# Kernel tuning notes

Measured on AMD Instinct MI355X. Metric: run time of the kernel, lower is better.

## Reference

```python
import jax, jax.numpy as jnp
import numpy as np

EMB = 1024
HEADS = 16

def setup_inputs() -> dict:
    key = jax.random.key(0)
    ks = jax.random.split(key, 5)
    s = 1.0 / np.sqrt(EMB)
    x = jax.random.normal(ks[0], (2, 2048, EMB), dtype=jnp.float32)
    W_qkv = jax.random.normal(ks[1], (EMB, 3 * EMB), dtype=jnp.float32) * s
    b_qkv = jnp.zeros((3 * EMB,), dtype=jnp.float32)
    W_out = jax.random.normal(ks[2], (EMB, EMB), dtype=jnp.float32) * s
    b_out = jnp.zeros((EMB,), dtype=jnp.float32)
    return {"x": x, "W_qkv": W_qkv, "b_qkv": b_qkv, "W_out": W_out, "b_out": b_out}

def reference(x, W_qkv, b_qkv, W_out, b_out):
    B, N, C = x.shape
    H = HEADS
    D = C // H
    qkv = x @ W_qkv + b_qkv                      # [B,N,3C]
    qkv = qkv.reshape(B, N, 3, H, D)
    q, k, v = (qkv[:, :, i].transpose(0, 2, 1, 3) for i in range(3))  # [B,H,N,D]
    # NOTE: original scales by C**-0.5 (full embed dim), not head dim
    scale = C ** (-0.5)
    attn = jnp.einsum('bhnd,bhmd->bhnm', q, k) * scale
    attn = jax.nn.softmax(attn, axis=-1)
    out = jnp.einsum('bhnm,bhmd->bhnd', attn, v)  # [B,H,N,D]
    out = out.transpose(0, 2, 1, 3).reshape(B, N, C)
    return out @ W_out + b_out
```

## Files before the change

### kernel.cpp

```cpp
#include <hip/hip_runtime.h>
#include <hip/hip_bf16.h>
#include <cstdint>
#include <cstddef>

typedef __bf16 bf16;
typedef __bf16 bf16x4 __attribute__((ext_vector_type(4)));
typedef __bf16 bf16x8 __attribute__((ext_vector_type(8)));
typedef float f32x4 __attribute__((ext_vector_type(4)));
typedef float f32x16 __attribute__((ext_vector_type(16)));

#define LOG2E 1.4426950408889634f
#define QSCALE (0.03125f * LOG2E)

#define GLD16(gp, lp)                                                              \
  __builtin_amdgcn_global_load_lds((__attribute__((address_space(1))) void*)(gp),  \
                                   (__attribute__((address_space(3))) void*)(lp),  \
                                   16, 0, 0)

__global__ void k_prep(const float* __restrict__ x, const float* __restrict__ Wqkv,
                       const float* __restrict__ Wout, bf16* __restrict__ xb,
                       bf16* __restrict__ wqT, bf16* __restrict__ woT) {
  const int blk = blockIdx.x, tid = threadIdx.x;
  if (blk < 2048) {
    int i = (blk * 256 + tid) * 8;
    const float4* p = (const float4*)(x + i);
    float4 a = p[0], b = p[1];
    bf16x8 o;
    o[0] = (bf16)a.x; o[1] = (bf16)a.y; o[2] = (bf16)a.z; o[3] = (bf16)a.w;
    o[4] = (bf16)b.x; o[5] = (bf16)b.y; o[6] = (bf16)b.z; o[7] = (bf16)b.w;
    *(bf16x8*)(xb + i) = o;
    return;
  }
  const float* in;
  bf16* out;
  int R = 1024, C, bx, by;
  if (blk < 2048 + 3072) {
    in = Wqkv; out = wqT; C = 3072;
    bx = (blk - 2048) % 96; by = (blk - 2048) / 96;
  } else {
    in = Wout; out = woT; C = 1024;
    bx = (blk - 5120) % 32; by = (blk - 5120) / 32;
  }
  __shared__ float t[32][33];
  const int tx = tid & 31, ty = tid >> 5;
  int c0 = bx * 32, r0 = by * 32;
#pragma unroll
  for (int i = 0; i < 4; i++)
    t[ty + i * 8][tx] = in[(size_t)(r0 + ty + i * 8) * C + c0 + tx];
  __syncthreads();
#pragma unroll
  for (int i = 0; i < 4; i++)
    out[(size_t)(c0 + ty + i * 8) * R + r0 + tx] = (bf16)t[tx][ty + i * 8];
}

__global__ __launch_bounds__(256, 3) void k_gemm_qkv(
    const bf16* __restrict__ A, const bf16* __restrict__ Bt,
    const float* __restrict__ bias,
    bf16* __restrict__ qb, bf16* __restrict__ kb, bf16* __restrict__ vb) {
  __shared__ __align__(16) bf16 As[128 * 32];
  __shared__ __align__(16) bf16 Bs[128 * 32];
  const int tid = threadIdx.x;
  const int lane = tid & 63, w = tid >> 6;
  const int quad = lane >> 4, l16 = lane & 15;
  const int wm = (w >> 1) * 64, wn = (w & 1) * 64;
  const int bm = blockIdx.y * 128, bn = blockIdx.x * 128;
  f32x4 acc[4][4] = {};

  for (int kt = 0; kt < 1024; kt += 32) {
    __syncthreads();
#pragma unroll
    for (int p = 0; p < 2; p++) {
      int idx = p * 256 + tid;
      int row = idx >> 2, bq = idx & 3;
      int gb = (bq - ((row >> 1) & 3)) & 3;
      GLD16(A + (size_t)(bm + row) * 1024 + kt + gb * 8, As + idx * 8);
      GLD16(Bt + (size_t)(bn + row) * 1024 + kt + gb * 8, Bs + idx * 8);
    }
    __syncthreads();

    bf16x8 af[4], bfr[4];
#pragma unroll
    for (int mi = 0; mi < 4; mi++) {
      int row = wm + mi * 16 + l16;
      int bq = (quad + ((row >> 1) & 3)) & 3;
      af[mi] = *(const bf16x8*)(As + row * 32 + bq * 8);
    }
#pragma unroll
    for (int ni = 0; ni < 4; ni++) {
      int row = wn + ni * 16 + l16;
      int bq = (quad + ((row >> 1) & 3)) & 3;
      bfr[ni] = *(const bf16x8*)(Bs + row * 32 + bq * 8);
    }
#pragma unroll
    for (int mi = 0; mi < 4; mi++)
#pragma unroll
      for (int ni = 0; ni < 4; ni++)
        acc[mi][ni] =
            __builtin_amdgcn_mfma_f32_16x16x32_bf16(af[mi], bfr[ni], acc[mi][ni], 0, 0, 0);
  }

#pragma unroll
  for (int ni = 0; ni < 4; ni++) {
    int col = bn + wn + ni * 16 + l16;
    float bv = bias[col];
    int which = col >> 10, cc = col & 1023;
    int h = cc >> 6, d = cc & 63;
    if (which == 2) {
#pragma unroll
      for (int mi = 0; mi < 4; mi++) {
        int rowb = bm + wm + mi * 16 + quad * 4;
        int b = rowb >> 11, n0 = rowb & 2047;
        int n0p = (n0 & ~12) | ((n0 & 4) << 1) | ((n0 & 8) >> 1);
        bf16x4 vv;
#pragma unroll
        for (int r = 0; r < 4; r++) vv[r] = (bf16)(acc[mi][ni][r] + bv);
        *(bf16x4*)(vb + ((size_t)(b * 16 + h) * 64 + d) * 2048 + n0p) = vv;
      }
    } else {
#pragma unroll
      for (int mi = 0; mi < 4; mi++)
#pragma unroll
        for (int r = 0; r < 4; r++) {
          int row = bm + wm + mi * 16 + quad * 4 + r;
          int b = row >> 11, n = row & 2047;
          float v = acc[mi][ni][r] + bv;
          if (which == 0)
            qb[((size_t)(b * 16 + h) * 2048 + n) * 64 + d] = (bf16)(v * QSCALE);
          else
            kb[((size_t)(b * 16 + h) * 2048 + n) * 64 + d] = (bf16)v;
        }
    }
  }
}

__global__ __launch_bounds__(256, 2) void k_gemm_out(
    const bf16* __restrict__ A, const bf16* __restrict__ Bt,
    const float* __restrict__ bias, float* __restrict__ outF) {
  __shared__ __align__(16) bf16 As[64 * 32];
  __shared__ __align__(16) bf16 Bs[128 * 32];
  const int tid = threadIdx.x;
  const int lane = tid & 63, w = tid >> 6;
  const int quad = lane >> 4, l16 = lane & 15;
  const int wm = (w >> 1) * 32, wn = (w & 1) * 64;
  const int cid = (blockIdx.x & 7) * 64 + (blockIdx.x >> 3);
  const int bn = (cid & 7) * 128, bm = (cid >> 3) * 64;
  f32x4 acc[2][4] = {};

  for (int kt = 0; kt < 1024; kt += 32) {
    __syncthreads();
    {
      int idx = tid;
      int row = idx >> 2, bq = idx & 3;
      int gb = (bq - ((row >> 1) & 3)) & 3;
      GLD16(A + (size_t)(bm + row) * 1024 + kt + gb * 8, As + idx * 8);
    }
#pragma unroll
    for (int p = 0; p < 2; p++) {
      int idx = p * 256 + tid;
      int row = idx >> 2, bq = idx & 3;
      int gb = (bq - ((row >> 1) & 3)) & 3;
      GLD16(Bt + (size_t)(bn + row) * 1024 + kt + gb * 8, Bs + idx * 8);
    }
    __syncthreads();

    bf16x8 af[2], bfr[4];
#pragma unroll
    for (int mi = 0; mi < 2; mi++) {
      int row = wm + mi * 16 + l16;
      int bq = (quad + ((row >> 1) & 3)) & 3;
      af[mi] = *(const bf16x8*)(As + row * 32 + bq * 8);
    }
#pragma unroll
    for (int ni = 0; ni < 4; ni++) {
      int row = wn + ni * 16 + l16;
      int bq = (quad + ((row >> 1) & 3)) & 3;
      bfr[ni] = *(const bf16x8*)(Bs + row * 32 + bq * 8);
    }
#pragma unroll
    for (int mi = 0; mi < 2; mi++)
#pragma unroll
      for (int ni = 0; ni < 4; ni++)
        acc[mi][ni] =
            __builtin_amdgcn_mfma_f32_16x16x32_bf16(af[mi], bfr[ni], acc[mi][ni], 0, 0, 0);
  }

#pragma unroll
  for (int ni = 0; ni < 4; ni++) {
    int col = bn + wn + ni * 16 + l16;
    float bv = bias[col];
#pragma unroll
    for (int mi = 0; mi < 2; mi++)
#pragma unroll
      for (int r = 0; r < 4; r++) {
        int row = bm + wm + mi * 16 + quad * 4 + r;
        outF[(size_t)row * 1024 + col] = acc[mi][ni][r] + bv;
      }
  }
}

__global__ __launch_bounds__(256, 2) void k_flash(
    const bf16* __restrict__ Q, const bf16* __restrict__ K,
    const bf16* __restrict__ V, bf16* __restrict__ O) {
  __shared__ __align__(16) bf16 Kt[2][128 * 64];
  __shared__ __align__(16) bf16 Vt[2][64 * 128];
  const int tid = threadIdx.x;
  const int lane = tid & 63, w = tid >> 6;
  const int l31 = lane & 31, h = lane >> 5;
  const int x7 = l31 & 7;
  const int cid = ((blockIdx.x & 7) << 6) | (blockIdx.x >> 3);
  const int qt = cid & 15, bh = cid >> 4;
  const bf16* qh = Q + (size_t)bh * 2048 * 64;
  const bf16* kh = K + (size_t)bh * 2048 * 64;
  const bf16* vh = V + (size_t)bh * 64 * 2048;
  const int qrow = qt * 128 + w * 32 + l31;

  bf16x8 qf[4];
#pragma unroll
  for (int c4 = 0; c4 < 4; c4++)
    qf[c4] = *(const bf16x8*)(qh + (size_t)qrow * 64 + c4 * 16 + h * 8);

  bf16x8 ones;
#pragma unroll
  for (int j = 0; j < 8; j++) ones[j] = (bf16)1.0f;
  f32x16 z16 = {};

  f32x16 o0 = {}, o1 = {};
  f32x16 lacc = {};

  auto stage = [&](int kt2, int buf) {
#pragma unroll
    for (int pp = 0; pp < 4; pp++) {
      int idx = pp * 256 + tid;
      int row = idx >> 3, bq = idx & 7, gb = bq ^ (row & 7);
      GLD16(kh + (size_t)(kt2 * 128 + row) * 64 + gb * 8, &Kt[buf][idx * 8]);
    }
#pragma unroll
    for (int pp = 0; pp < 4; pp++) {
      int idx = pp * 256 + tid;
      int row = idx >> 4, bq = idx & 15, gb = bq ^ (row & 7);
      GLD16(vh + (size_t)row * 2048 + kt2 * 128 + gb * 8, &Vt[buf][idx * 8]);
    }
  };

  stage(0, 0);

  for (int t = 0; t < 16; t++) {
    const int p = t & 1;
    __syncthreads();
    if (t < 15) stage(t + 1, p ^ 1);
    const bf16* Kb = &Kt[p][0];
    const bf16* Vb = &Vt[p][0];

    f32x16 a[4];
    {
      __builtin_amdgcn_s_setprio(1);
#pragma unroll
      for (int c4 = 0; c4 < 4; c4++) {
        int off = ((2 * c4 + h) ^ x7) << 3;
#pragma unroll
        for (int g = 0; g < 4; g++) {
          bf16x8 kf = *(const bf16x8*)(Kb + (g * 32 + l31) * 64 + off);
          a[g] = __builtin_amdgcn_mfma_f32_32x32x16_bf16(kf, qf[c4], c4 ? a[g] : z16,
                                                         0, 0, 0);
        }
      }
      __builtin_amdgcn_s_setprio(0);
    }

    const bf16* v0 = Vb + l31 * 128;
    const bf16* v1 = v0 + 32 * 128;

#pragma unroll
    for (int g = 0; g < 4; g++) {
      bf16x8 pf0, pf1;
#pragma unroll
      for (int j = 0; j < 8; j++) {
        pf0[j] = (bf16)__builtin_amdgcn_exp2f(a[g][j]);
        pf1[j] = (bf16)__builtin_amdgcn_exp2f(a[g][8 + j]);
      }
      int e0 = ((4 * g + 0 + h) ^ x7) << 3;
      int e1 = ((4 * g + 2 + h) ^ x7) << 3;
      bf16x8 vf00 = *(const bf16x8*)(v0 + e0);
      bf16x8 vf10 = *(const bf16x8*)(v1 + e0);
      bf16x8 vf01 = *(const bf16x8*)(v0 + e1);
      bf16x8 vf11 = *(const bf16x8*)(v1 + e1);
      __builtin_amdgcn_s_setprio(1);
      lacc = __builtin_amdgcn_mfma_f32_32x32x16_bf16(ones, pf0, lacc, 0, 0, 0);
      o0 = __builtin_amdgcn_mfma_f32_32x32x16_bf16(vf00, pf0, o0, 0, 0, 0);
      o1 = __builtin_amdgcn_mfma_f32_32x32x16_bf16(vf10, pf0, o1, 0, 0, 0);
      lacc = __builtin_amdgcn_mfma_f32_32x32x16_bf16(ones, pf1, lacc, 0, 0, 0);
      o0 = __builtin_amdgcn_mfma_f32_32x32x16_bf16(vf01, pf1, o0, 0, 0, 0);
      o1 = __builtin_amdgcn_mfma_f32_32x32x16_bf16(vf11, pf1, o1, 0, 0, 0);
      __builtin_amdgcn_s_setprio(0);
    }
  }

  float inv = 1.0f / lacc[0];
  const int bb = bh >> 4, hh = bh & 15;
  bf16* orow = O + ((size_t)bb * 2048 + qrow) * 1024 + hh * 64;
#pragma unroll
  for (int g = 0; g < 4; g++) {
    bf16x4 ov0, ov1;
#pragma unroll
    for (int r = 0; r < 4; r++) {
      ov0[r] = (bf16)(o0[4 * g + r] * inv);
      ov1[r] = (bf16)(o1[4 * g + r] * inv);
    }
    *(bf16x4*)(orow + 8 * g + 4 * h) = ov0;
    *(bf16x4*)(orow + 32 + 8 * g + 4 * h) = ov1;
  }
}


extern "C" void kernel_launch(void* const* d_in, const int* in_sizes, int n_in,
                              void* d_out, int out_size, void* d_ws, size_t ws_size,
                              hipStream_t stream) {
  (void)in_sizes; (void)n_in; (void)out_size; (void)ws_size;
  const float* x    = (const float*)d_in[0];
  const float* Wqkv = (const float*)d_in[1];
  const float* bqkv = (const float*)d_in[2];
  const float* Wout = (const float*)d_in[3];
  const float* bout = (const float*)d_in[4];
  float* out = (float*)d_out;

  char* ws = (char*)d_ws;
  size_t off = 0;
  auto take = [&](size_t bytes) {
    char* p = ws + off;
    off += (bytes + 255) & ~(size_t)255;
    return p;
  };
  bf16* xb   = (bf16*)take((size_t)4096 * 1024 * 2);
  bf16* wqT  = (bf16*)take((size_t)3072 * 1024 * 2);
  bf16* woT  = (bf16*)take((size_t)1024 * 1024 * 2);
  bf16* qbuf = (bf16*)take((size_t)32 * 2048 * 64 * 2);
  bf16* kbuf = (bf16*)take((size_t)32 * 2048 * 64 * 2);
  bf16* vbuf = (bf16*)take((size_t)32 * 2048 * 64 * 2);
  bf16* aout = (bf16*)take((size_t)4096 * 1024 * 2);

  k_prep<<<6144, 256, 0, stream>>>(x, Wqkv, Wout, xb, wqT, woT);
  k_gemm_qkv<<<dim3(24, 32), 256, 0, stream>>>(xb, wqT, bqkv, qbuf, kbuf, vbuf);
  k_flash<<<dim3(512), 256, 0, stream>>>(qbuf, kbuf, vbuf, aout);
  k_gemm_out<<<dim3(512), 256, 0, stream>>>(aout, woT, bout, out);
}
```

Baseline: 180.4 us.

## Split flash attention KV range across warp pairs with LDS reduction

Each block now covers 64 query rows instead of 128. Its four waves form two query groups times two KV halves: each wave takes 32 keys of every 64-key tile, and the partial outputs and row sums are combined through shared memory at the end. Tiles and shared memory are halved, the grid doubles to 1024 blocks, and launch bounds rise to 4 blocks per CU to improve occupancy and latency hiding. In exchange, K/V traffic per query roughly doubles, there are twice as many barrier iterations, and an extra reduction step is added.

```diff
diff --git a/kernel.cpp b/kernel.cpp
--- a/kernel.cpp
+++ b/kernel.cpp
@@ -198,21 +198,22 @@
   }
 }
 
-__global__ __launch_bounds__(256, 2) void k_flash(
+__global__ __launch_bounds__(256, 4) void k_flash(
     const bf16* __restrict__ Q, const bf16* __restrict__ K,
     const bf16* __restrict__ V, bf16* __restrict__ O) {
-  __shared__ __align__(16) bf16 Kt[2][128 * 64];
-  __shared__ __align__(16) bf16 Vt[2][64 * 128];
+  __shared__ __align__(16) bf16 Kt[2][64 * 64];
+  __shared__ __align__(16) bf16 Vt[2][64 * 64];
   const int tid = threadIdx.x;
   const int lane = tid & 63, w = tid >> 6;
+  const int wq = w >> 1, wk = w & 1;
   const int l31 = lane & 31, h = lane >> 5;
   const int x7 = l31 & 7;
-  const int cid = ((blockIdx.x & 7) << 6) | (blockIdx.x >> 3);
-  const int qt = cid & 15, bh = cid >> 4;
+  const int cid = ((blockIdx.x & 7) << 7) | (blockIdx.x >> 3);
+  const int qt = cid & 31, bh = cid >> 5;
   const bf16* qh = Q + (size_t)bh * 2048 * 64;
   const bf16* kh = K + (size_t)bh * 2048 * 64;
   const bf16* vh = V + (size_t)bh * 64 * 2048;
-  const int qrow = qt * 128 + w * 32 + l31;
+  const int qrow = qt * 64 + wq * 32 + l31;
 
   bf16x8 qf[4];
 #pragma unroll
@@ -229,57 +230,45 @@
 
   auto stage = [&](int kt2, int buf) {
 #pragma unroll
-    for (int pp = 0; pp < 4; pp++) {
+    for (int pp = 0; pp < 2; pp++) {
       int idx = pp * 256 + tid;
       int row = idx >> 3, bq = idx & 7, gb = bq ^ (row & 7);
-      GLD16(kh + (size_t)(kt2 * 128 + row) * 64 + gb * 8, &Kt[buf][idx * 8]);
-    }
-#pragma unroll
-    for (int pp = 0; pp < 4; pp++) {
-      int idx = pp * 256 + tid;
-      int row = idx >> 4, bq = idx & 15, gb = bq ^ (row & 7);
-      GLD16(vh + (size_t)row * 2048 + kt2 * 128 + gb * 8, &Vt[buf][idx * 8]);
+      GLD16(kh + (size_t)(kt2 * 64 + row) * 64 + gb * 8, &Kt[buf][idx * 8]);
+      GLD16(vh + (size_t)row * 2048 + kt2 * 64 + gb * 8, &Vt[buf][idx * 8]);
     }
   };
 
   stage(0, 0);
 
-  for (int t = 0; t < 16; t++) {
+  for (int t = 0; t < 32; t++) {
     const int p = t & 1;
     __syncthreads();
-    if (t < 15) stage(t + 1, p ^ 1);
-    const bf16* Kb = &Kt[p][0];
-    const bf16* Vb = &Vt[p][0];
-
-    f32x16 a[4];
+    if (t < 31) stage(t + 1, p ^ 1);
+
+    f32x16 a;
     {
+      const bf16* k0 = &Kt[p][0] + (wk * 32 + l31) * 64;
       __builtin_amdgcn_s_setprio(1);
 #pragma unroll
       for (int c4 = 0; c4 < 4; c4++) {
         int off = ((2 * c4 + h) ^ x7) << 3;
-#pragma unroll
-        for (int g = 0; g < 4; g++) {
-          bf16x8 kf = *(const bf16x8*)(Kb + (g * 32 + l31) * 64 + off);
-          a[g] = __builtin_amdgcn_mfma_f32_32x32x16_bf16(kf, qf[c4], c4 ? a[g] : z16,
-                                                         0, 0, 0);
-        }
+        bf16x8 kf = *(const bf16x8*)(k0 + off);
+        a = __builtin_amdgcn_mfma_f32_32x32x16_bf16(kf, qf[c4], c4 ? a : z16, 0, 0, 0);
       }
       __builtin_amdgcn_s_setprio(0);
     }
 
-    const bf16* v0 = Vb + l31 * 128;
-    const bf16* v1 = v0 + 32 * 128;
-
-#pragma unroll
-    for (int g = 0; g < 4; g++) {
+    {
       bf16x8 pf0, pf1;
 #pragma unroll
       for (int j = 0; j < 8; j++) {
-        pf0[j] = (bf16)__builtin_amdgcn_exp2f(a[g][j]);
-        pf1[j] = (bf16)__builtin_amdgcn_exp2f(a[g][8 + j]);
-      }
-      int e0 = ((4 * g + 0 + h) ^ x7) << 3;
-      int e1 = ((4 * g + 2 + h) ^ x7) << 3;
+        pf0[j] = (bf16)__builtin_amdgcn_exp2f(a[j]);
+        pf1[j] = (bf16)__builtin_amdgcn_exp2f(a[8 + j]);
+      }
+      const bf16* v0 = &Vt[p][0] + l31 * 64;
+      const bf16* v1 = v0 + 32 * 64;
+      int e0 = ((4 * wk + 0 + h) ^ x7) << 3;
+      int e1 = ((4 * wk + 2 + h) ^ x7) << 3;
       bf16x8 vf00 = *(const bf16x8*)(v0 + e0);
       bf16x8 vf10 = *(const bf16x8*)(v1 + e0);
       bf16x8 vf01 = *(const bf16x8*)(v0 + e1);
@@ -295,19 +284,38 @@
     }
   }
 
-  float inv = 1.0f / lacc[0];
-  const int bb = bh >> 4, hh = bh & 15;
-  bf16* orow = O + ((size_t)bb * 2048 + qrow) * 1024 + hh * 64;
-#pragma unroll
-  for (int g = 0; g < 4; g++) {
-    bf16x4 ov0, ov1;
-#pragma unroll
-    for (int r = 0; r < 4; r++) {
-      ov0[r] = (bf16)(o0[4 * g + r] * inv);
-      ov1[r] = (bf16)(o1[4 * g + r] * inv);
-    }
-    *(bf16x4*)(orow + 8 * g + 4 * h) = ov0;
-    *(bf16x4*)(orow + 32 + 8 * g + 4 * h) = ov1;
+  __syncthreads();
+  float* sc = (float*)&Kt[0][0];
+  float* so0 = sc;
+  float* so1 = sc + 2 * 64 * 17;
+  float* sl  = sc + 4 * 64 * 17;
+  if (wk == 1) {
+    float* b0 = so0 + (wq * 64 + lane) * 17;
+    float* b1 = so1 + (wq * 64 + lane) * 17;
+#pragma unroll
+    for (int i = 0; i < 16; i++) { b0[i] = o0[i]; b1[i] = o1[i]; }
+    sl[wq * 64 + lane] = lacc[0];
+  }
+  __syncthreads();
+  if (wk == 0) {
+    float* b0 = so0 + (wq * 64 + lane) * 17;
+    float* b1 = so1 + (wq * 64 + lane) * 17;
+#pragma unroll
+    for (int i = 0; i < 16; i++) { o0[i] += b0[i]; o1[i] += b1[i]; }
+    float inv = 1.0f / (lacc[0] + sl[wq * 64 + lane]);
+    const int bb = bh >> 4, hh = bh & 15;
+    bf16* orow = O + ((size_t)bb * 2048 + qrow) * 1024 + hh * 64;
+#pragma unroll
+    for (int g = 0; g < 4; g++) {
+      bf16x4 ov0, ov1;
+#pragma unroll
+      for (int r = 0; r < 4; r++) {
+        ov0[r] = (bf16)(o0[4 * g + r] * inv);
+        ov1[r] = (bf16)(o1[4 * g + r] * inv);
+      }
+      *(bf16x4*)(orow + 8 * g + 4 * h) = ov0;
+      *(bf16x4*)(orow + 32 + 8 * g + 4 * h) = ov1;
+    }
   }
 }
 
@@ -340,6 +348,6 @@
 
   k_prep<<<6144, 256, 0, stream>>>(x, Wqkv, Wout, xb, wqT, woT);
   k_gemm_qkv<<<dim3(24, 32), 256, 0, stream>>>(xb, wqT, bqkv, qbuf, kbuf, vbuf);
-  k_flash<<<dim3(512), 256, 0, stream>>>(qbuf, kbuf, vbuf, aout);
+  k_flash<<<dim3(1024), 256, 0, stream>>>(qbuf, kbuf, vbuf, aout);
   k_gemm_out<<<dim3(512), 256, 0, stream>>>(aout, woT, bout, out);
 }
```

Result: slower. 186.6 us (+3.4%).
